# Kernel tuning notes

Hardware: AMD Instinct MI355X
Metric: run time of the kernel (lower is better)

## Reference

```python
import jax, jax.numpy as jnp
import numpy as np

# DAttentionBaseline config (matches init_kwargs)
NH, HC, G = 8, 32, 4          # n_heads, n_head_channels, n_groups
ORF = 2.0                      # offset_range_factor
KK = 5                         # offset conv kernel (stage_idx=2)


def _conv1x1(x, w, b=None):
    # x: (B,C,H,W), w: (O,C)
    y = jnp.einsum('bchw,oc->bohw', x, w)
    return y if b is None else y + b[None, :, None, None]


def _ref_points(Hk, Wk, dtype):
    # replicates torch.meshgrid(..., indexing='xy') as in the source
    ly = jnp.linspace(0.5, Hk - 0.5, Hk, dtype=dtype)
    lx = jnp.linspace(0.5, Wk - 0.5, Wk, dtype=dtype)
    ry, rx = jnp.meshgrid(ly, lx, indexing='xy')  # shapes (Wk, Hk); Hk==Wk here
    return jnp.stack([ry / Hk * 2 - 1, rx / Wk * 2 - 1], axis=-1)  # (Hk,Wk,2)


def _grid_sample(img, grid):
    # bilinear, align_corners=True, zero padding. img:(N,C,Hi,Wi), grid:(N,Hg,Wg,2) in [-1,1] (x,y)
    N, C, Hi, Wi = img.shape
    gx = (grid[..., 0] + 1.0) * 0.5 * (Wi - 1)
    gy = (grid[..., 1] + 1.0) * 0.5 * (Hi - 1)
    x0 = jnp.floor(gx); y0 = jnp.floor(gy)
    x1 = x0 + 1.0;      y1 = y0 + 1.0
    wx1 = gx - x0; wx0 = 1.0 - wx1
    wy1 = gy - y0; wy0 = 1.0 - wy1
    nidx = jnp.arange(N)[:, None, None]

    def gather(yf, xf):
        valid = (xf >= 0) & (xf <= Wi - 1) & (yf >= 0) & (yf <= Hi - 1)
        xi = jnp.clip(xf, 0, Wi - 1).astype(jnp.int32)
        yi = jnp.clip(yf, 0, Hi - 1).astype(jnp.int32)
        vals = img[nidx, :, yi, xi]  # (N,Hg,Wg,C)
        return vals * valid[..., None].astype(img.dtype)

    out = (gather(y0, x0) * (wy0 * wx0)[..., None]
           + gather(y0, x1) * (wy0 * wx1)[..., None]
           + gather(y1, x0) * (wy1 * wx0)[..., None]
           + gather(y1, x1) * (wy1 * wx1)[..., None])
    return out.transpose(0, 3, 1, 2)  # (N,C,Hg,Wg)


def _forward(x, wq, bq, w_off_dw, b_off_dw, ln_g, ln_b, w_off_pj, wk, bk, wv, bv, wo, bo, rpe_table):
    B, C, H, W = x.shape
    GC = C // G            # group channels
    GH = NH // G           # group heads
    scale = HC ** -0.5

    q = _conv1x1(x, wq, bq)                                   # (B,C,H,W)
    q_off = q.reshape(B * G, GC, H, W)

    # conv_offset: depthwise conv -> LayerNorm over channels -> GELU -> 1x1 conv to 2
    off = jax.lax.conv_general_dilated(
        q_off, w_off_dw, (1, 1), [(KK // 2, KK // 2), (KK // 2, KK // 2)],
        feature_group_count=GC, dimension_numbers=('NCHW', 'OIHW', 'NCHW'))
    off = off + b_off_dw[None, :, None, None]
    mu = off.mean(axis=1, keepdims=True)
    var = off.var(axis=1, keepdims=True)
    off = (off - mu) * jax.lax.rsqrt(var + 1e-5)
    off = off * ln_g[None, :, None, None] + ln_b[None, :, None, None]
    off = jax.nn.gelu(off, approximate=False)
    offset = jnp.einsum('bchw,oc->bohw', off, w_off_pj)       # (B*G,2,Hk,Wk)

    Hk, Wk = offset.shape[2], offset.shape[3]
    ns = Hk * Wk
    rng = jnp.array([1.0 / Hk, 1.0 / Wk], dtype=x.dtype).reshape(1, 2, 1, 1)
    offset = jnp.tanh(offset) * rng * ORF                     # offset_range_factor > 0
    offset = offset.transpose(0, 2, 3, 1)                     # (B*G,Hk,Wk,2)

    ref = _ref_points(Hk, Wk, x.dtype)                        # (Hk,Wk,2)
    pos = offset + ref[None]                                  # (B*G,Hk,Wk,2), (y,x) order

    xs = _grid_sample(x.reshape(B * G, GC, H, W), pos[..., ::-1])  # (B*G,GC,Hk,Wk)
    xs = xs.reshape(B, C, 1, ns)

    k = _conv1x1(xs, wk, bk).reshape(B * NH, HC, ns)
    v = _conv1x1(xs, wv, bv).reshape(B * NH, HC, ns)
    qf = q.reshape(B * NH, HC, H * W)
    attn = jnp.einsum('bcm,bcn->bmn', qf, k) * scale          # (B*NH, HW, ns)

    # RPE via grid_sample on the (2H-1, 2W-1) bias table
    rpe = jnp.broadcast_to(rpe_table[None], (B,) + rpe_table.shape)
    rpe = rpe.reshape(B * G, GH, 2 * H - 1, 2 * W - 1)
    qg = _ref_points(H, W, x.dtype).reshape(H * W, 2)
    disp = (qg[None, :, None, :] - pos.reshape(B * G, ns, 2)[:, None, :, :]) * 0.5  # (B*G,HW,ns,2)
    bias = _grid_sample(rpe, disp[..., ::-1]).reshape(B * NH, H * W, ns)
    attn = attn + bias

    attn = jax.nn.softmax(attn, axis=2)
    out = jnp.einsum('bmn,bcn->bcm', attn, v).reshape(B, C, H, W)
    y = _conv1x1(out, wo, bo)
    return (y,
            pos.reshape(B, G, Hk, Wk, 2),
            jnp.broadcast_to(ref[None, None], (B, G, Hk, Wk, 2)))


def setup_inputs() -> dict:
    key = jax.random.key(0)
    ks = jax.random.split(key, 8)
    B, C, H, W = 4, 256, 32, 32
    GC = C // G
    s = 0.02

    def n(k, shape, sc=s):
        return jax.random.normal(k, shape, jnp.float32) * sc

    return {
        'x': jax.random.normal(ks[0], (B, C, H, W), jnp.float32),
        'wq': n(ks[1], (C, C)), 'bq': jnp.zeros((C,), jnp.float32),
        'w_off_dw': n(ks[2], (GC, 1, KK, KK)), 'b_off_dw': jnp.zeros((GC,), jnp.float32),
        'ln_g': jnp.ones((GC,), jnp.float32), 'ln_b': jnp.zeros((GC,), jnp.float32),
        'w_off_pj': n(ks[3], (2, GC)),
        'wk': n(ks[4], (C, C)), 'bk': jnp.zeros((C,), jnp.float32),
        'wv': n(ks[5], (C, C)), 'bv': jnp.zeros((C,), jnp.float32),
        'wo': n(ks[6], (C, C)), 'bo': jnp.zeros((C,), jnp.float32),
        'rpe_table': n(ks[7], (NH, 2 * H - 1, 2 * W - 1), 0.01),
    }


def reference(x, wq, bq, w_off_dw, b_off_dw, ln_g, ln_b, w_off_pj, wk, bk, wv, bv, wo, bo, rpe_table):
    return _forward(x, wq, bq, w_off_dw, b_off_dw, ln_g, ln_b, w_off_pj, wk, bk, wv, bv, wo, bo, rpe_table)
```

## Files before the change

kernel.cpp:

```cpp
#include <hip/hip_runtime.h>
#include <math.h>

#define CK __restrict__

constexpr int CH = 256;
constexpr int HW = 1024;

typedef __attribute__((ext_vector_type(8))) short short8;
typedef __attribute__((ext_vector_type(4))) float f32x4;

__device__ __forceinline__ ushort f2b(float x) {
    union { float f; unsigned int u; } a; a.f = x;
    unsigned int r = (a.u + 0x7FFFu + ((a.u >> 16) & 1u)) >> 16;
    return (ushort)r;
}
__device__ __forceinline__ short8 ld8(const ushort* p) { return *(const short8*)p; }
__device__ __forceinline__ float u2f(unsigned int u) {
    union { unsigned int u; float f; } a; a.u = u; return a.f;
}
__device__ __forceinline__ float b2f(ushort us) { return u2f((unsigned int)us << 16); }

__global__ __launch_bounds__(256) void prep(const float* CK w0, const float* CK w1,
                                            const float* CK w2, const float* CK w3,
                                            ushort* CK o0, ushort* CK o1,
                                            ushort* CK o2, ushort* CK o3,
                                            const float* CK x, ushort* CK xT,
                                            const float* CK rpe, unsigned int* CK rpetab) {
    const int bid = blockIdx.x, t = threadIdx.x;
    if (bid < 256) {
        const float* src; ushort* dst;
        switch (bid >> 6) {
            case 0: src = w0; dst = o0; break;
            case 1: src = w1; dst = o1; break;
            case 2: src = w2; dst = o2; break;
            default: src = w3; dst = o3; break;
        }
        const int i = (bid & 63) * 256 + t;
        float4 v = ((const float4*)src)[i];
        ushort4 r; r.x = f2b(v.x); r.y = f2b(v.y); r.z = f2b(v.z); r.w = f2b(v.w);
        ((ushort4*)dst)[i] = r;
    } else if (bid < 384) {
        const int b2 = bid - 256;
        const int c8 = b2 & 31, b = b2 >> 5;
        for (int nn = 0; nn < 4; nn++) {
            const int n = nn * 256 + t;
            union { ushort u[8]; short8 s; } pk;
#pragma unroll
            for (int j = 0; j < 8; j++) pk.u[j] = f2b(x[(b * 256 + c8 * 8 + j) * HW + n]);
            *(short8*)(xT + b * 262144 + n * 256 + c8 * 8) = pk.s;
        }
    } else {
        const int h = bid - 384;
        const float* rp = rpe + h * 3969;
        unsigned int* dst = rpetab + h * 4356;
        for (int i = t; i < 4356; i += 256) {
            int y = i / 67, x2 = i - y * 67;
            int yy = y - 1, xx = x2 - 1;
            bool vy = (yy >= 0) && (yy < 63) && (y < 65);
            float a  = (vy && xx >= 0 && xx < 63) ? rp[yy * 63 + xx] : 0.f;
            float bb = (vy && xx >= -1 && xx < 62) ? rp[yy * 63 + xx + 1] : 0.f;
            dst[i] = (unsigned int)f2b(a) | ((unsigned int)f2b(bb) << 16);
        }
    }
}

__global__ __launch_bounds__(256) void gemm_q(const ushort* CK AT, const ushort* CK W,
                                              const float* CK bias, ushort* CK Y) {
    const int b = blockIdx.z;
    const int t = threadIdx.x, w = t >> 6, l = t & 63;
    const int lm = l & 15, qd = l >> 4;
    const int m0 = blockIdx.y * 64 + (w & 1) * 32;
    const int n0 = blockIdx.x * 64 + (w >> 1) * 32;
    const ushort* A = AT + b * 262144 + n0 * 256;
    const ushort* Bm = W + m0 * 256;
    f32x4 acc[2][2] = {};
#pragma unroll
    for (int k0 = 0; k0 < 8; k0++) {
        const int ko = k0 * 32 + qd * 8;
        short8 a0 = ld8(A + lm * 256 + ko);
        short8 a1 = ld8(A + (16 + lm) * 256 + ko);
        short8 b0 = ld8(Bm + lm * 256 + ko);
        short8 b1 = ld8(Bm + (16 + lm) * 256 + ko);
        acc[0][0] = __builtin_amdgcn_mfma_f32_16x16x32_bf16(a0, b0, acc[0][0], 0, 0, 0);
        acc[0][1] = __builtin_amdgcn_mfma_f32_16x16x32_bf16(a0, b1, acc[0][1], 0, 0, 0);
        acc[1][0] = __builtin_amdgcn_mfma_f32_16x16x32_bf16(a1, b0, acc[1][0], 0, 0, 0);
        acc[1][1] = __builtin_amdgcn_mfma_f32_16x16x32_bf16(a1, b1, acc[1][1], 0, 0, 0);
    }
#pragma unroll
    for (int in = 0; in < 2; in++)
#pragma unroll
        for (int im = 0; im < 2; im++) {
            const int m = m0 + im * 16 + lm;
            const float bs = bias[m];
            ushort4 r;
            r.x = f2b(acc[in][im][0] + bs); r.y = f2b(acc[in][im][1] + bs);
            r.z = f2b(acc[in][im][2] + bs); r.w = f2b(acc[in][im][3] + bs);
            *(ushort4*)(Y + b * 262144 + m * HW + n0 + in * 16 + qd * 4) = r;
        }
}

__global__ __launch_bounds__(256) void gemm_o(const ushort* CK AT, const ushort* CK W,
                                              const float* CK bias, float* CK Y) {
    const int b = blockIdx.z;
    const int t = threadIdx.x, w = t >> 6, l = t & 63;
    const int lm = l & 15, qd = l >> 4;
    const int m0 = blockIdx.y * 64 + (w & 1) * 32;
    const int n0 = blockIdx.x * 64 + (w >> 1) * 32;
    const ushort* A = AT + b * 262144 + n0 * 256;
    const ushort* Bm = W + m0 * 256;
    f32x4 acc[2][2] = {};
#pragma unroll
    for (int k0 = 0; k0 < 8; k0++) {
        const int ko = k0 * 32 + qd * 8;
        short8 a0 = ld8(A + lm * 256 + ko);
        short8 a1 = ld8(A + (16 + lm) * 256 + ko);
        short8 b0 = ld8(Bm + lm * 256 + ko);
        short8 b1 = ld8(Bm + (16 + lm) * 256 + ko);
        acc[0][0] = __builtin_amdgcn_mfma_f32_16x16x32_bf16(a0, b0, acc[0][0], 0, 0, 0);
        acc[0][1] = __builtin_amdgcn_mfma_f32_16x16x32_bf16(a0, b1, acc[0][1], 0, 0, 0);
        acc[1][0] = __builtin_amdgcn_mfma_f32_16x16x32_bf16(a1, b0, acc[1][0], 0, 0, 0);
        acc[1][1] = __builtin_amdgcn_mfma_f32_16x16x32_bf16(a1, b1, acc[1][1], 0, 0, 0);
    }
#pragma unroll
    for (int in = 0; in < 2; in++)
#pragma unroll
        for (int im = 0; im < 2; im++) {
            const int m = m0 + im * 16 + lm;
            const float bs = bias[m];
            float4 r;
            r.x = acc[in][im][0] + bs; r.y = acc[in][im][1] + bs;
            r.z = acc[in][im][2] + bs; r.w = acc[in][im][3] + bs;
            *(float4*)(Y + b * 262144 + m * HW + n0 + in * 16 + qd * 4) = r;
        }
}

__global__ __launch_bounds__(256) void gemm_kv(const ushort* CK AT,
                                               const ushort* CK Wk, const float* CK bk, ushort* CK kbt,
                                               const ushort* CK Wv, const float* CK bv, ushort* CK vbs) {
    const int b = blockIdx.z;
    const int t = threadIdx.x, w = t >> 6, l = t & 63;
    const int lm = l & 15, qd = l >> 4;
    const int m0 = blockIdx.y * 64 + (w & 1) * 32;
    const int n0 = blockIdx.x * 64 + (w >> 1) * 32;
    const ushort* A = AT + b * 262144 + n0 * 256;
    const ushort* Bk = Wk + m0 * 256;
    const ushort* Bv = Wv + m0 * 256;
    f32x4 akT[2][2] = {}, av[2][2] = {};
#pragma unroll
    for (int k0 = 0; k0 < 8; k0++) {
        const int ko = k0 * 32 + qd * 8;
        short8 a0 = ld8(A + lm * 256 + ko);
        short8 a1 = ld8(A + (16 + lm) * 256 + ko);
        short8 k0f = ld8(Bk + lm * 256 + ko);
        short8 k1f = ld8(Bk + (16 + lm) * 256 + ko);
        short8 v0f = ld8(Bv + lm * 256 + ko);
        short8 v1f = ld8(Bv + (16 + lm) * 256 + ko);
        akT[0][0] = __builtin_amdgcn_mfma_f32_16x16x32_bf16(k0f, a0, akT[0][0], 0, 0, 0);
        akT[0][1] = __builtin_amdgcn_mfma_f32_16x16x32_bf16(k0f, a1, akT[0][1], 0, 0, 0);
        akT[1][0] = __builtin_amdgcn_mfma_f32_16x16x32_bf16(k1f, a0, akT[1][0], 0, 0, 0);
        akT[1][1] = __builtin_amdgcn_mfma_f32_16x16x32_bf16(k1f, a1, akT[1][1], 0, 0, 0);
        av[0][0] = __builtin_amdgcn_mfma_f32_16x16x32_bf16(a0, v0f, av[0][0], 0, 0, 0);
        av[0][1] = __builtin_amdgcn_mfma_f32_16x16x32_bf16(a0, v1f, av[0][1], 0, 0, 0);
        av[1][0] = __builtin_amdgcn_mfma_f32_16x16x32_bf16(a1, v0f, av[1][0], 0, 0, 0);
        av[1][1] = __builtin_amdgcn_mfma_f32_16x16x32_bf16(a1, v1f, av[1][1], 0, 0, 0);
    }
#pragma unroll
    for (int im = 0; im < 2; im++)
#pragma unroll
        for (int in = 0; in < 2; in++) {
            {
                const int c0 = m0 + im * 16 + qd * 4;
                const int n  = n0 + in * 16 + lm;
                const int bh = b * 8 + (c0 >> 5);
                const int qdk = (c0 & 31) >> 3, co4 = c0 & 7;
                const int nc = n >> 7, nbk = (n >> 4) & 7, lmk = n & 15;
                const float4 bks = *(const float4*)(bk + c0);
                ushort4 r4;
                r4.x = f2b(akT[im][in][0] + bks.x);
                r4.y = f2b(akT[im][in][1] + bks.y);
                r4.z = f2b(akT[im][in][2] + bks.z);
                r4.w = f2b(akT[im][in][3] + bks.w);
                *(ushort4*)(kbt + ((bh * 8 + nc) * 512 + nbk * 64 + qdk * 16 + lmk) * 8 + co4) = r4;
            }
            {
                const int c = m0 + im * 16 + lm;
                const int bh = b * 8 + (c >> 5);
                const float bs = bv[c];
                const int cb = (c & 31) >> 4, lmv = c & 15;
                const int nbase = n0 + in * 16 + qd * 4;
                const int nc = nbase >> 7, kc = (nbase >> 5) & 3;
                const int qdv = (nbase >> 3) & 3, co0 = nbase & 7;
                ushort4 r4;
                r4.x = f2b(av[in][im][0] + bs); r4.y = f2b(av[in][im][1] + bs);
                r4.z = f2b(av[in][im][2] + bs); r4.w = f2b(av[in][im][3] + bs);
                *(ushort4*)(vbs + ((bh * 8 + nc) * 512 + (cb * 4 + kc) * 64 + qdv * 16 + lmv) * 8 + co0) = r4;
            }
        }
}

__global__ __launch_bounds__(256) void dwconv(const ushort* CK q, const float* CK wdw,
                                              const float* CK bdw, float* CK off) {
    const int bx = blockIdx.x;
    const int ch = bx & 63;
    const ushort* qb = q + bx * HW;
    float w[25];
#pragma unroll
    for (int i = 0; i < 25; i++) w[i] = wdw[ch * 25 + i];
    const float bb = bdw[ch];
    const int t = threadIdx.x;
#pragma unroll
    for (int p = 0; p < 4; p++) {
        int hw = p * 256 + t;
        int ii = hw >> 5, jj = hw & 31;
        float s = bb;
#pragma unroll
        for (int ky = 0; ky < 5; ky++) {
            int y = ii + ky - 2;
            if (y < 0 || y > 31) continue;
#pragma unroll
            for (int kx = 0; kx < 5; kx++) {
                int x = jj + kx - 2;
                if (x < 0 || x > 31) continue;
                s += b2f(qb[y * 32 + x]) * w[ky * 5 + kx];
            }
        }
        off[bx * HW + hw] = s;
    }
}

__global__ __launch_bounds__(256) void lnps(const float* CK off, const float* CK ln_g,
                                            const float* CK ln_b, const float* CK wpj,
                                            const float* CK x,
                                            float* CK out_pos, float* CK out_ref,
                                            float2* CK pos_sc, ushort* CK xsT) {
    const int bid = blockIdx.x, t = threadIdx.x;
    const int bg = bid >> 4;
    const int pix_l = t >> 2, qtr = t & 3;
    const int n = (bid & 15) * 64 + pix_l;
    const int gid = bg * 1024 + n;
    const float* ob = off + bg * 64 * HW + n;
    const int c0 = qtr * 16;
    float v[16];
    float s1 = 0.f;
#pragma unroll
    for (int j = 0; j < 16; j++) { v[j] = ob[(c0 + j) * HW]; s1 += v[j]; }
    s1 += __shfl_xor(s1, 1); s1 += __shfl_xor(s1, 2);
    const float mean = s1 * 0.015625f;
    float s2 = 0.f;
#pragma unroll
    for (int j = 0; j < 16; j++) { float d = v[j] - mean; s2 += d * d; }
    s2 += __shfl_xor(s2, 1); s2 += __shfl_xor(s2, 2);
    const float rs = rsqrtf(s2 * 0.015625f + 1e-5f);
    float p0 = 0.f, p1 = 0.f;
#pragma unroll
    for (int j = 0; j < 16; j++) {
        float vv = (v[j] - mean) * rs * ln_g[c0 + j] + ln_b[c0 + j];
        float gl = 0.5f * vv * (1.f + erff(vv * 0.70710678118654752f));
        p0 += gl * wpj[c0 + j];
        p1 += gl * wpj[64 + c0 + j];
    }
    p0 += __shfl_xor(p0, 1); p0 += __shfl_xor(p0, 2);
    p1 += __shfl_xor(p1, 1); p1 += __shfl_xor(p1, 2);
    const int ii = n >> 5, jj = n & 31;
    const float r0 = (jj + 0.5f) * 0.0625f - 1.f;
    const float r1 = (ii + 0.5f) * 0.0625f - 1.f;
    const float pos0 = tanhf(p0) * 0.0625f + r0;
    const float pos1 = tanhf(p1) * 0.0625f + r1;
    if (qtr == 0) {
        out_pos[gid * 2] = pos0; out_pos[gid * 2 + 1] = pos1;
        out_ref[gid * 2] = r0;   out_ref[gid * 2 + 1] = r1;
        pos_sc[gid].x = pos0 * 15.5f; pos_sc[gid].y = pos1 * 15.5f;
    }
    const float gx = (pos1 + 1.f) * 15.5f, gy = (pos0 + 1.f) * 15.5f;
    const float x0f = floorf(gx), y0f = floorf(gy);
    const float wx1 = gx - x0f, wx0 = 1.f - wx1, wy1 = gy - y0f, wy0 = 1.f - wy1;
    const bool vx0 = (x0f >= 0.f) && (x0f <= 31.f);
    const bool vx1 = (x0f >= -1.f) && (x0f <= 30.f);
    const bool vy0 = (y0f >= 0.f) && (y0f <= 31.f);
    const bool vy1 = (y0f >= -1.f) && (y0f <= 30.f);
    const int xi0 = (int)fminf(fmaxf(x0f, 0.f), 31.f);
    const int xi1 = (int)fminf(fmaxf(x0f + 1.f, 0.f), 31.f);
    const int yi0 = (int)fminf(fmaxf(y0f, 0.f), 31.f);
    const int yi1 = (int)fminf(fmaxf(y0f + 1.f, 0.f), 31.f);
    const float w00 = (vy0 && vx0) ? wy0 * wx0 : 0.f;
    const float w01 = (vy0 && vx1) ? wy0 * wx1 : 0.f;
    const float w10 = (vy1 && vx0) ? wy1 * wx0 : 0.f;
    const float w11 = (vy1 && vx1) ? wy1 * wx1 : 0.f;
    const int o00 = yi0 * 32 + xi0, o01 = yi0 * 32 + xi1;
    const int o10 = yi1 * 32 + xi0, o11 = yi1 * 32 + xi1;
    const int b = bg >> 2, g = bg & 3;
    const float* xb = x + bg * 64 * HW;
    ushort* xo = xsT + b * 262144 + n * 256 + g * 64 + c0;
#pragma unroll
    for (int j4 = 0; j4 < 4; j4++) {
        ushort4 r4;
        float vals[4];
#pragma unroll
        for (int j = 0; j < 4; j++) {
            const float* p = xb + (c0 + j4 * 4 + j) * HW;
            vals[j] = w00 * p[o00] + w01 * p[o01] + w10 * p[o10] + w11 * p[o11];
        }
        r4.x = f2b(vals[0]); r4.y = f2b(vals[1]); r4.z = f2b(vals[2]); r4.w = f2b(vals[3]);
        *(ushort4*)(xo + j4 * 4) = r4;
    }
}

__global__ __launch_bounds__(256, 7) void attn_part(const ushort* CK q, const ushort* CK kbt,
                                                    const ushort* CK vbs, const float2* CK pos_sc,
                                                    const unsigned int* CK rpetab,
                                                    ushort* CK partO, float2* CK mlbuf) {
    __shared__ __align__(16) unsigned int rpe_pr[4356];
    __shared__ __align__(16) ushort Pl[4][544];
    const int bh = blockIdx.y, quarter = blockIdx.z;
    const int b = bh >> 3, nh = bh & 7, bg = bh >> 1;
    const int t = threadIdx.x;
    const int w = t >> 6, l = t & 63;
    const int lm = l & 15, qd = l >> 4;

    {
        const uint4* src4 = (const uint4*)(rpetab + nh * 4356);
        uint4* dst4 = (uint4*)rpe_pr;
        for (int i = t; i < 1089; i += 256) dst4[i] = src4[i];
    }
    __syncthreads();

    const int m = blockIdx.x * 64 + w * 16 + lm;
    short8 qf;
    {
        union { ushort u[8]; short8 s; } pk;
        const ushort* qb = q + (b * 256 + nh * 32) * HW + m;
#pragma unroll
        for (int j = 0; j < 8; j++) pk.u[j] = qb[(qd * 8 + j) * HW];
        qf = pk.s;
    }
    const float qg0 = ((m & 31) + 0.5f) * 0.0625f - 1.f;
    const float qg1 = ((m >> 5) + 0.5f) * 0.0625f - 1.f;
    const float ax = 31.f + 15.5f * qg1;
    const float ay = 31.f + 15.5f * qg0;

    f32x4 oacc0 = {0.f, 0.f, 0.f, 0.f}, oacc1 = {0.f, 0.f, 0.f, 0.f};
    float rmax = -3e38f, rsum = 0.f;
    ushort* PlW = Pl[w];
    const float2* pbase = pos_sc + bg * 1024;

    for (int nc = quarter * 2; nc < quarter * 2 + 2; nc++) {
        const ushort* kg = kbt + (bh * 8 + nc) * 4096;
        const ushort* vg = vbs + (bh * 8 + nc) * 4096;

#pragma unroll
        for (int nb2 = 0; nb2 < 4; nb2++) {
            f32x4 sT[2];
#pragma unroll
            for (int s = 0; s < 2; s++) {
                const int nb = nb2 * 2 + s;
                sT[s] = __builtin_amdgcn_mfma_f32_16x16x32_bf16(
                            ld8(kg + (nb * 64 + l) * 8), qf,
                            (f32x4){0.f, 0.f, 0.f, 0.f}, 0, 0, 0);
            }
            float cmax = -3e38f;
#pragma unroll
            for (int s = 0; s < 2; s++) {
                const float4* pp = (const float4*)(pbase + nc * 128 + (nb2 * 2 + s) * 16 + qd * 4);
                const float4 pa = pp[0], pb_ = pp[1];
                const float psx[4] = {pa.x, pa.z, pb_.x, pb_.z};
                const float psy[4] = {pa.y, pa.w, pb_.y, pb_.w};
#pragma unroll
                for (int r = 0; r < 4; r++) {
                    const float gx = ax - psy[r];
                    const float gy = ay - psx[r];
                    const float x0f = floorf(gx), y0f = floorf(gy);
                    const float wx1 = gx - x0f, wy1 = gy - y0f;
                    const int idx = (int)y0f * 67 + (int)x0f + 68;
                    const unsigned int pr0 = rpe_pr[idx];
                    const unsigned int pr1 = rpe_pr[idx + 67];
                    const float t00 = u2f(pr0 << 16), t01 = u2f(pr0 & 0xFFFF0000u);
                    const float t10 = u2f(pr1 << 16), t11 = u2f(pr1 & 0xFFFF0000u);
                    const float u0 = t00 + wx1 * (t01 - t00);
                    const float u1 = t10 + wx1 * (t11 - t10);
                    sT[s][r] = sT[s][r] * 0.17677669529663687f + (u0 + wy1 * (u1 - u0));
                    cmax = fmaxf(cmax, sT[s][r]);
                }
            }
            cmax = fmaxf(cmax, __shfl_xor(cmax, 16));
            cmax = fmaxf(cmax, __shfl_xor(cmax, 32));
            const float newmax = fmaxf(rmax, cmax);
            const float alpha = __expf(rmax - newmax);
            rmax = newmax;
            float csum = 0.f;
#pragma unroll
            for (int s = 0; s < 2; s++) {
                float e0 = __expf(sT[s][0] - rmax);
                float e1 = __expf(sT[s][1] - rmax);
                float e2 = __expf(sT[s][2] - rmax);
                float e3 = __expf(sT[s][3] - rmax);
                csum += (e0 + e1) + (e2 + e3);
                uint2 pk;
                pk.x = (unsigned int)f2b(e0) | ((unsigned int)f2b(e1) << 16);
                pk.y = (unsigned int)f2b(e2) | ((unsigned int)f2b(e3) << 16);
                *(uint2*)(PlW + s * 272 + l * 4) = pk;
            }
            csum += __shfl_xor(csum, 16);
            csum += __shfl_xor(csum, 32);
            rsum = rsum * alpha + csum;
            oacc0 *= alpha;
            oacc1 *= alpha;
            const ushort* pb2 = PlW + (qd >> 1) * 272 + (qd & 1) * 128 + lm * 4;
            union { uint2 u[2]; short8 s; } pfu;
            pfu.u[0] = *(const uint2*)pb2;
            pfu.u[1] = *(const uint2*)(pb2 + 64);
            oacc0 = __builtin_amdgcn_mfma_f32_16x16x32_bf16(ld8(vg + (nb2 * 64 + l) * 8), pfu.s, oacc0, 0, 0, 0);
            oacc1 = __builtin_amdgcn_mfma_f32_16x16x32_bf16(ld8(vg + ((4 + nb2) * 64 + l) * 8), pfu.s, oacc1, 0, 0, 0);
        }
    }

    ushort* po = partO + (((quarter * 32 + bh) * 1024 + m) * 32) + qd * 4;
    ushort4 r04, r14;
    r04.x = f2b(oacc0[0]); r04.y = f2b(oacc0[1]); r04.z = f2b(oacc0[2]); r04.w = f2b(oacc0[3]);
    r14.x = f2b(oacc1[0]); r14.y = f2b(oacc1[1]); r14.z = f2b(oacc1[2]); r14.w = f2b(oacc1[3]);
    *(ushort4*)po = r04;
    *(ushort4*)(po + 16) = r14;
    if (qd == 0) {
        float2 ml; ml.x = rmax; ml.y = rsum;
        mlbuf[(quarter * 32 + bh) * 1024 + m] = ml;
    }
}

__global__ __launch_bounds__(128) void attn_comb(const ushort* CK partO, const float2* CK mlbuf,
                                                 ushort* CK aoT) {
    const int gid = blockIdx.x * 128 + threadIdx.x;
    const int bh = gid >> 10, m = gid & 1023;
    const int b = bh >> 3, nh = bh & 7;
    float2 ml[4];
    float M = -3e38f;
#pragma unroll
    for (int i = 0; i < 4; i++) { ml[i] = mlbuf[(i * 32 + bh) * 1024 + m]; M = fmaxf(M, ml[i].x); }
    float e[4], denom = 0.f;
#pragma unroll
    for (int i = 0; i < 4; i++) { e[i] = __expf(ml[i].x - M); denom += ml[i].y * e[i]; }
    const float inv = 1.f / denom;
#pragma unroll
    for (int i = 0; i < 4; i++) e[i] *= inv;
    ushort* ob = aoT + b * 262144 + m * 256 + nh * 32;
#pragma unroll
    for (int g8 = 0; g8 < 4; g8++) {
        float acc[8] = {};
#pragma unroll
        for (int i = 0; i < 4; i++) {
            union { ushort u[8]; short8 s; } pv;
            pv.s = ld8(partO + ((i * 32 + bh) * 1024 + m) * 32 + g8 * 8);
#pragma unroll
            for (int j = 0; j < 8; j++) acc[j] += b2f(pv.u[j]) * e[i];
        }
        union { ushort u[8]; short8 s; } o;
#pragma unroll
        for (int j = 0; j < 8; j++) o.u[j] = f2b(acc[j]);
        *(short8*)(ob + g8 * 8) = o.s;
    }
}

extern "C" void kernel_launch(void* const* d_in, const int* in_sizes, int n_in,
                              void* d_out, int out_size, void* d_ws, size_t ws_size,
                              hipStream_t stream) {
    (void)in_sizes; (void)n_in; (void)out_size; (void)ws_size;
    const float* x   = (const float*)d_in[0];
    const float* wq  = (const float*)d_in[1];
    const float* bq  = (const float*)d_in[2];
    const float* wdw = (const float*)d_in[3];
    const float* bdw = (const float*)d_in[4];
    const float* lng = (const float*)d_in[5];
    const float* lnb = (const float*)d_in[6];
    const float* wpj = (const float*)d_in[7];
    const float* wk  = (const float*)d_in[8];
    const float* bk  = (const float*)d_in[9];
    const float* wv  = (const float*)d_in[10];
    const float* bv  = (const float*)d_in[11];
    const float* wo  = (const float*)d_in[12];
    const float* bo  = (const float*)d_in[13];
    const float* rpe = (const float*)d_in[14];
    float* outp = (float*)d_out;
    char* base = (char*)d_ws;
    const size_t MB = 1 << 20;

    ushort* q_b    = (ushort*)(base);
    ushort* kbt    = (ushort*)(base + 2 * MB);
    ushort* vbs    = (ushort*)(base + 4 * MB);
    float*  off_ws = (float*)(base + 6 * MB);
    ushort* xT     = (ushort*)(base + 10 * MB);
    ushort* xsT    = (ushort*)(base + 12 * MB);
    ushort* partO  = (ushort*)(base + 6 * MB);
    float2* mlbuf  = (float2*)(base + 14 * MB);
    ushort* aoT    = (ushort*)(base + 15 * MB);
    ushort* wqb    = (ushort*)(base + 17 * MB);
    ushort* wkb    = (ushort*)(base + 17 * MB + 131072);
    ushort* wvb    = (ushort*)(base + 17 * MB + 262144);
    ushort* wob    = (ushort*)(base + 17 * MB + 393216);
    float2* pos_sc = (float2*)(base + 17 * MB + 524288);
    unsigned int* rpetab = (unsigned int*)(base + 17 * MB + 655360);

    prep<<<392, 256, 0, stream>>>(wq, wk, wv, wo, wqb, wkb, wvb, wob, x, xT, rpe, rpetab);
    gemm_q<<<dim3(16, 4, 4), 256, 0, stream>>>(xT, wqb, bq, q_b);
    dwconv<<<1024, 256, 0, stream>>>(q_b, wdw, bdw, off_ws);
    lnps<<<256, 256, 0, stream>>>(off_ws, lng, lnb, wpj, x,
                                  outp + (1 << 20), outp + (1 << 20) + 32768, pos_sc, xsT);
    gemm_kv<<<dim3(16, 4, 4), 256, 0, stream>>>(xsT, wkb, bk, kbt, wvb, bv, vbs);
    attn_part<<<dim3(16, 32, 4), 256, 0, stream>>>(q_b, kbt, vbs, pos_sc, rpetab, partO, mlbuf);
    attn_comb<<<256, 128, 0, stream>>>(partO, mlbuf, aoT);
    gemm_o<<<dim3(16, 4, 4), 256, 0, stream>>>(aoT, wob, bo, outp);
}
```

Measured before the change: 188.8 us.

## Fuse split-softmax combine into output projection GEMM and widen attention chunk

Removes the separate attn_comb kernel. The output GEMM now rescales and sums the four partial attention outputs on the fly while building its A fragments, with the softmax weights held in shared memory. This saves one launch and the aoT round trip through memory, at the cost of recomputing the combine in each of the four blocks along the output-channel dimension. The attention kernel also processes 64 keys per softmax step instead of 32 (larger P tile, occupancy hint lowered from 7 to 4) and computes the RPE bilinear bias on paired vector floats using truncation instead of floor.

```diff
diff --git a/kernel.cpp b/kernel.cpp
--- a/kernel.cpp
+++ b/kernel.cpp
@@ -8,6 +8,7 @@
 
 typedef __attribute__((ext_vector_type(8))) short short8;
 typedef __attribute__((ext_vector_type(4))) float f32x4;
+typedef __attribute__((ext_vector_type(2))) float v2f;
 
 __device__ __forceinline__ ushort f2b(float x) {
     union { float f; unsigned int u; } a; a.f = x;
@@ -96,41 +97,6 @@
             r.x = f2b(acc[in][im][0] + bs); r.y = f2b(acc[in][im][1] + bs);
             r.z = f2b(acc[in][im][2] + bs); r.w = f2b(acc[in][im][3] + bs);
             *(ushort4*)(Y + b * 262144 + m * HW + n0 + in * 16 + qd * 4) = r;
-        }
-}
-
-__global__ __launch_bounds__(256) void gemm_o(const ushort* CK AT, const ushort* CK W,
-                                              const float* CK bias, float* CK Y) {
-    const int b = blockIdx.z;
-    const int t = threadIdx.x, w = t >> 6, l = t & 63;
-    const int lm = l & 15, qd = l >> 4;
-    const int m0 = blockIdx.y * 64 + (w & 1) * 32;
-    const int n0 = blockIdx.x * 64 + (w >> 1) * 32;
-    const ushort* A = AT + b * 262144 + n0 * 256;
-    const ushort* Bm = W + m0 * 256;
-    f32x4 acc[2][2] = {};
-#pragma unroll
-    for (int k0 = 0; k0 < 8; k0++) {
-        const int ko = k0 * 32 + qd * 8;
-        short8 a0 = ld8(A + lm * 256 + ko);
-        short8 a1 = ld8(A + (16 + lm) * 256 + ko);
-        short8 b0 = ld8(Bm + lm * 256 + ko);
-        short8 b1 = ld8(Bm + (16 + lm) * 256 + ko);
-        acc[0][0] = __builtin_amdgcn_mfma_f32_16x16x32_bf16(a0, b0, acc[0][0], 0, 0, 0);
-        acc[0][1] = __builtin_amdgcn_mfma_f32_16x16x32_bf16(a0, b1, acc[0][1], 0, 0, 0);
-        acc[1][0] = __builtin_amdgcn_mfma_f32_16x16x32_bf16(a1, b0, acc[1][0], 0, 0, 0);
-        acc[1][1] = __builtin_amdgcn_mfma_f32_16x16x32_bf16(a1, b1, acc[1][1], 0, 0, 0);
-    }
-#pragma unroll
-    for (int in = 0; in < 2; in++)
-#pragma unroll
-        for (int im = 0; im < 2; im++) {
-            const int m = m0 + im * 16 + lm;
-            const float bs = bias[m];
-            float4 r;
-            r.x = acc[in][im][0] + bs; r.y = acc[in][im][1] + bs;
-            r.z = acc[in][im][2] + bs; r.w = acc[in][im][3] + bs;
-            *(float4*)(Y + b * 262144 + m * HW + n0 + in * 16 + qd * 4) = r;
         }
 }
 
@@ -305,12 +271,12 @@
     }
 }
 
-__global__ __launch_bounds__(256, 7) void attn_part(const ushort* CK q, const ushort* CK kbt,
+__global__ __launch_bounds__(256, 4) void attn_part(const ushort* CK q, const ushort* CK kbt,
                                                     const ushort* CK vbs, const float2* CK pos_sc,
                                                     const unsigned int* CK rpetab,
                                                     ushort* CK partO, float2* CK mlbuf) {
     __shared__ __align__(16) unsigned int rpe_pr[4356];
-    __shared__ __align__(16) ushort Pl[4][544];
+    __shared__ __align__(16) ushort Pl[4][1088];
     const int bh = blockIdx.y, quarter = blockIdx.z;
     const int b = bh >> 3, nh = bh & 7, bg = bh >> 1;
     const int t = threadIdx.x;
@@ -348,37 +314,45 @@
         const ushort* vg = vbs + (bh * 8 + nc) * 4096;
 
 #pragma unroll
-        for (int nb2 = 0; nb2 < 4; nb2++) {
-            f32x4 sT[2];
-#pragma unroll
-            for (int s = 0; s < 2; s++) {
-                const int nb = nb2 * 2 + s;
+        for (int g = 0; g < 2; g++) {
+            f32x4 sT[4];
+#pragma unroll
+            for (int s = 0; s < 4; s++) {
+                const int nb = g * 4 + s;
                 sT[s] = __builtin_amdgcn_mfma_f32_16x16x32_bf16(
                             ld8(kg + (nb * 64 + l) * 8), qf,
                             (f32x4){0.f, 0.f, 0.f, 0.f}, 0, 0, 0);
             }
             float cmax = -3e38f;
 #pragma unroll
-            for (int s = 0; s < 2; s++) {
-                const float4* pp = (const float4*)(pbase + nc * 128 + (nb2 * 2 + s) * 16 + qd * 4);
+            for (int s = 0; s < 4; s++) {
+                const float4* pp = (const float4*)(pbase + nc * 128 + (g * 4 + s) * 16 + qd * 4);
                 const float4 pa = pp[0], pb_ = pp[1];
                 const float psx[4] = {pa.x, pa.z, pb_.x, pb_.z};
                 const float psy[4] = {pa.y, pa.w, pb_.y, pb_.w};
 #pragma unroll
-                for (int r = 0; r < 4; r++) {
-                    const float gx = ax - psy[r];
-                    const float gy = ay - psx[r];
-                    const float x0f = floorf(gx), y0f = floorf(gy);
-                    const float wx1 = gx - x0f, wy1 = gy - y0f;
-                    const int idx = (int)y0f * 67 + (int)x0f + 68;
-                    const unsigned int pr0 = rpe_pr[idx];
-                    const unsigned int pr1 = rpe_pr[idx + 67];
-                    const float t00 = u2f(pr0 << 16), t01 = u2f(pr0 & 0xFFFF0000u);
-                    const float t10 = u2f(pr1 << 16), t11 = u2f(pr1 & 0xFFFF0000u);
-                    const float u0 = t00 + wx1 * (t01 - t00);
-                    const float u1 = t10 + wx1 * (t11 - t10);
-                    sT[s][r] = sT[s][r] * 0.17677669529663687f + (u0 + wy1 * (u1 - u0));
-                    cmax = fmaxf(cmax, sT[s][r]);
+                for (int rp = 0; rp < 2; rp++) {
+                    v2f gx = {ax - psy[rp * 2], ax - psy[rp * 2 + 1]};
+                    v2f gy = {ay - psx[rp * 2], ay - psx[rp * 2 + 1]};
+                    const int xi0 = (int)gx.x, xi1 = (int)gx.y;
+                    const int yi0 = (int)gy.x, yi1 = (int)gy.y;
+                    v2f wx = gx - (v2f){(float)xi0, (float)xi1};
+                    v2f wy = gy - (v2f){(float)yi0, (float)yi1};
+                    const int idxA = yi0 * 67 + xi0 + 68;
+                    const int idxB = yi1 * 67 + xi1 + 68;
+                    const unsigned int a0 = rpe_pr[idxA], a1 = rpe_pr[idxA + 67];
+                    const unsigned int b0 = rpe_pr[idxB], b1 = rpe_pr[idxB + 67];
+                    v2f tA = {u2f(a0 << 16), u2f(a0 & 0xFFFF0000u)};
+                    v2f bA = {u2f(a1 << 16), u2f(a1 & 0xFFFF0000u)};
+                    v2f tB = {u2f(b0 << 16), u2f(b0 & 0xFFFF0000u)};
+                    v2f bB = {u2f(b1 << 16), u2f(b1 & 0xFFFF0000u)};
+                    v2f vA = tA + wy.x * (bA - tA);
+                    v2f vB = tB + wy.y * (bB - tB);
+                    const float biasA = vA.x + wx.x * (vA.y - vA.x);
+                    const float biasB = vB.x + wx.y * (vB.y - vB.x);
+                    sT[s][rp * 2]     = sT[s][rp * 2]     * 0.17677669529663687f + biasA;
+                    sT[s][rp * 2 + 1] = sT[s][rp * 2 + 1] * 0.17677669529663687f + biasB;
+                    cmax = fmaxf(cmax, fmaxf(sT[s][rp * 2], sT[s][rp * 2 + 1]));
                 }
             }
             cmax = fmaxf(cmax, __shfl_xor(cmax, 16));
@@ -388,7 +362,7 @@
             rmax = newmax;
             float csum = 0.f;
 #pragma unroll
-            for (int s = 0; s < 2; s++) {
+            for (int s = 0; s < 4; s++) {
                 float e0 = __expf(sT[s][0] - rmax);
                 float e1 = __expf(sT[s][1] - rmax);
                 float e2 = __expf(sT[s][2] - rmax);
@@ -404,12 +378,16 @@
             rsum = rsum * alpha + csum;
             oacc0 *= alpha;
             oacc1 *= alpha;
-            const ushort* pb2 = PlW + (qd >> 1) * 272 + (qd & 1) * 128 + lm * 4;
-            union { uint2 u[2]; short8 s; } pfu;
-            pfu.u[0] = *(const uint2*)pb2;
-            pfu.u[1] = *(const uint2*)(pb2 + 64);
-            oacc0 = __builtin_amdgcn_mfma_f32_16x16x32_bf16(ld8(vg + (nb2 * 64 + l) * 8), pfu.s, oacc0, 0, 0, 0);
-            oacc1 = __builtin_amdgcn_mfma_f32_16x16x32_bf16(ld8(vg + ((4 + nb2) * 64 + l) * 8), pfu.s, oacc1, 0, 0, 0);
+#pragma unroll
+            for (int kc = 0; kc < 2; kc++) {
+                const ushort* pb2 = PlW + (kc * 2 + (qd >> 1)) * 272 + (qd & 1) * 128 + lm * 4;
+                union { uint2 u[2]; short8 s; } pfu;
+                pfu.u[0] = *(const uint2*)pb2;
+                pfu.u[1] = *(const uint2*)(pb2 + 64);
+                const int kv = g * 2 + kc;
+                oacc0 = __builtin_amdgcn_mfma_f32_16x16x32_bf16(ld8(vg + (kv * 64 + l) * 8), pfu.s, oacc0, 0, 0, 0);
+                oacc1 = __builtin_amdgcn_mfma_f32_16x16x32_bf16(ld8(vg + ((4 + kv) * 64 + l) * 8), pfu.s, oacc1, 0, 0, 0);
+            }
         }
     }
 
@@ -425,37 +403,81 @@
     }
 }
 
-__global__ __launch_bounds__(128) void attn_comb(const ushort* CK partO, const float2* CK mlbuf,
-                                                 ushort* CK aoT) {
-    const int gid = blockIdx.x * 128 + threadIdx.x;
-    const int bh = gid >> 10, m = gid & 1023;
-    const int b = bh >> 3, nh = bh & 7;
-    float2 ml[4];
-    float M = -3e38f;
-#pragma unroll
-    for (int i = 0; i < 4; i++) { ml[i] = mlbuf[(i * 32 + bh) * 1024 + m]; M = fmaxf(M, ml[i].x); }
-    float e[4], denom = 0.f;
-#pragma unroll
-    for (int i = 0; i < 4; i++) { e[i] = __expf(ml[i].x - M); denom += ml[i].y * e[i]; }
-    const float inv = 1.f / denom;
-#pragma unroll
-    for (int i = 0; i < 4; i++) e[i] *= inv;
-    ushort* ob = aoT + b * 262144 + m * 256 + nh * 32;
-#pragma unroll
-    for (int g8 = 0; g8 < 4; g8++) {
-        float acc[8] = {};
-#pragma unroll
-        for (int i = 0; i < 4; i++) {
-            union { ushort u[8]; short8 s; } pv;
-            pv.s = ld8(partO + ((i * 32 + bh) * 1024 + m) * 32 + g8 * 8);
-#pragma unroll
-            for (int j = 0; j < 8; j++) acc[j] += b2f(pv.u[j]) * e[i];
-        }
-        union { ushort u[8]; short8 s; } o;
-#pragma unroll
-        for (int j = 0; j < 8; j++) o.u[j] = f2b(acc[j]);
-        *(short8*)(ob + g8 * 8) = o.s;
-    }
+__global__ __launch_bounds__(256) void gemm_oc(const ushort* CK partO, const float2* CK mlbuf,
+                                               const ushort* CK W, const float* CK bias,
+                                               float* CK Y) {
+    __shared__ __align__(16) float ew[64][8][4];
+    const int b = blockIdx.z;
+    const int t = threadIdx.x, w = t >> 6, l = t & 63;
+    const int lm = l & 15, qd = l >> 4;
+    const int m0 = blockIdx.y * 64 + (w & 1) * 32;
+    const int n0 = blockIdx.x * 64 + (w >> 1) * 32;
+    const int nblk = blockIdx.x * 64;
+
+    for (int p = t; p < 512; p += 256) {
+        const int pix = p >> 3, head = p & 7;
+        const int mg = nblk + pix;
+        const int bh = b * 8 + head;
+        float2 ml[4];
+        float M = -3e38f;
+#pragma unroll
+        for (int q2 = 0; q2 < 4; q2++) {
+            ml[q2] = mlbuf[(q2 * 32 + bh) * 1024 + mg];
+            M = fmaxf(M, ml[q2].x);
+        }
+        float e[4], den = 0.f;
+#pragma unroll
+        for (int q2 = 0; q2 < 4; q2++) { e[q2] = __expf(ml[q2].x - M); den += ml[q2].y * e[q2]; }
+        const float inv = 1.f / den;
+#pragma unroll
+        for (int q2 = 0; q2 < 4; q2++) ew[pix][head][q2] = e[q2] * inv;
+    }
+    __syncthreads();
+
+    const ushort* Bm = W + m0 * 256;
+    f32x4 acc[2][2] = {};
+#pragma unroll
+    for (int k0 = 0; k0 < 8; k0++) {
+        const int ko = k0 * 32 + qd * 8;
+        short8 af[2];
+#pragma unroll
+        for (int half = 0; half < 2; half++) {
+            const int pix_l = (w >> 1) * 32 + half * 16 + lm;
+            const int mg = nblk + pix_l;
+            const ushort* pbq = partO + ((b * 8 + k0) * 1024 + mg) * 32 + qd * 8;
+            const float4 e4 = *(const float4*)&ew[pix_l][k0][0];
+            float a8[8] = {};
+#pragma unroll
+            for (int q2 = 0; q2 < 4; q2++) {
+                union { ushort u[8]; short8 s; } pv;
+                pv.s = ld8(pbq + q2 * 1048576);
+                const float eq = (q2 == 0) ? e4.x : (q2 == 1) ? e4.y : (q2 == 2) ? e4.z : e4.w;
+#pragma unroll
+                for (int j = 0; j < 8; j++) a8[j] += b2f(pv.u[j]) * eq;
+            }
+            union { ushort u[8]; short8 s; } out;
+#pragma unroll
+            for (int j = 0; j < 8; j++) out.u[j] = f2b(a8[j]);
+            af[half] = out.s;
+        }
+        short8 b0 = ld8(Bm + lm * 256 + ko);
+        short8 b1 = ld8(Bm + (16 + lm) * 256 + ko);
+        acc[0][0] = __builtin_amdgcn_mfma_f32_16x16x32_bf16(af[0], b0, acc[0][0], 0, 0, 0);
+        acc[0][1] = __builtin_amdgcn_mfma_f32_16x16x32_bf16(af[0], b1, acc[0][1], 0, 0, 0);
+        acc[1][0] = __builtin_amdgcn_mfma_f32_16x16x32_bf16(af[1], b0, acc[1][0], 0, 0, 0);
+        acc[1][1] = __builtin_amdgcn_mfma_f32_16x16x32_bf16(af[1], b1, acc[1][1], 0, 0, 0);
+    }
+#pragma unroll
+    for (int in = 0; in < 2; in++)
+#pragma unroll
+        for (int im = 0; im < 2; im++) {
+            const int mo = m0 + im * 16 + lm;
+            const float bs = bias[mo];
+            float4 r;
+            r.x = acc[in][im][0] + bs; r.y = acc[in][im][1] + bs;
+            r.z = acc[in][im][2] + bs; r.w = acc[in][im][3] + bs;
+            *(float4*)(Y + b * 262144 + mo * HW + n0 + in * 16 + qd * 4) = r;
+        }
 }
 
 extern "C" void kernel_launch(void* const* d_in, const int* in_sizes, int n_in,
@@ -489,13 +511,12 @@
     ushort* xsT    = (ushort*)(base + 12 * MB);
     ushort* partO  = (ushort*)(base + 6 * MB);
     float2* mlbuf  = (float2*)(base + 14 * MB);
-    ushort* aoT    = (ushort*)(base + 15 * MB);
-    ushort* wqb    = (ushort*)(base + 17 * MB);
-    ushort* wkb    = (ushort*)(base + 17 * MB + 131072);
-    ushort* wvb    = (ushort*)(base + 17 * MB + 262144);
-    ushort* wob    = (ushort*)(base + 17 * MB + 393216);
-    float2* pos_sc = (float2*)(base + 17 * MB + 524288);
-    unsigned int* rpetab = (unsigned int*)(base + 17 * MB + 655360);
+    ushort* wqb    = (ushort*)(base + 15 * MB);
+    ushort* wkb    = (ushort*)(base + 15 * MB + 131072);
+    ushort* wvb    = (ushort*)(base + 15 * MB + 262144);
+    ushort* wob    = (ushort*)(base + 15 * MB + 393216);
+    float2* pos_sc = (float2*)(base + 15 * MB + 524288);
+    unsigned int* rpetab = (unsigned int*)(base + 15 * MB + 655360);
 
     prep<<<392, 256, 0, stream>>>(wq, wk, wv, wo, wqb, wkb, wvb, wob, x, xT, rpe, rpetab);
     gemm_q<<<dim3(16, 4, 4), 256, 0, stream>>>(xT, wqb, bq, q_b);
@@ -504,6 +525,5 @@
                                   outp + (1 << 20), outp + (1 << 20) + 32768, pos_sc, xsT);
     gemm_kv<<<dim3(16, 4, 4), 256, 0, stream>>>(xsT, wkb, bk, kbt, wvb, bv, vbs);
     attn_part<<<dim3(16, 32, 4), 256, 0, stream>>>(q_b, kbt, vbs, pos_sc, rpetab, partO, mlbuf);
-    attn_comb<<<256, 128, 0, stream>>>(partO, mlbuf, aoT);
-    gemm_o<<<dim3(16, 4, 4), 256, 0, stream>>>(aoT, wob, bo, outp);
-}
+    gemm_oc<<<dim3(16, 4, 4), 256, 0, stream>>>(partO, mlbuf, wob, bo, outp);
+}
```

New measurement: 182.5 us. 3.3% less time.
